# Kernel optimization log

Hardware: AMD Instinct MI355X
Metric: run time of the kernel (lower is better)

## Reference

```python
import jax, jax.numpy as jnp
import numpy as np

HIDDEN = 256
INPUT = 128
B, T = 256, 512
W_SCALE = 1.0 / np.sqrt(HIDDEN)  # matches PyTorch U(-1/sqrt(H), 1/sqrt(H)) magnitude


def setup_inputs() -> dict:
    key = jax.random.key(0)
    ks = jax.random.split(key, 5)
    x = jax.random.normal(ks[0], (B, T, INPUT), dtype=jnp.float32)
    W_ih = jax.random.normal(ks[1], (3 * HIDDEN, INPUT), dtype=jnp.float32) * W_SCALE
    W_hh = jax.random.normal(ks[2], (3 * HIDDEN, HIDDEN), dtype=jnp.float32) * W_SCALE
    b_ih = jax.random.normal(ks[3], (3 * HIDDEN,), dtype=jnp.float32) * W_SCALE
    b_hh = jax.random.normal(ks[4], (3 * HIDDEN,), dtype=jnp.float32) * W_SCALE
    return {"x": x, "W_ih": W_ih, "W_hh": W_hh, "b_ih": b_ih, "b_hh": b_hh}


def reference(x, W_ih, W_hh, b_ih, b_hh):
    # PyTorch GRU, gate order (r, z, n):
    #   r = sigmoid(W_ir x + b_ir + W_hr h + b_hr)
    #   z = sigmoid(W_iz x + b_iz + W_hz h + b_hz)
    #   n = tanh(W_in x + b_in + r * (W_hn h + b_hn))
    #   h' = (1 - z) * n + z * h
    Bsz = x.shape[0]
    H = W_hh.shape[1]
    # Precompute all input-to-gate projections once (big GEMM outside the scan).
    xg = jnp.einsum('bti,gi->btg', x, W_ih) + b_ih  # [B, T, 3H]

    def step(h, xg_t):
        hg = h @ W_hh.T + b_hh                      # [B, 3H]
        xr, xz, xn = jnp.split(xg_t, 3, axis=-1)
        hr, hz, hn = jnp.split(hg, 3, axis=-1)
        r = jax.nn.sigmoid(xr + hr)
        z = jax.nn.sigmoid(xz + hz)
        n = jnp.tanh(xn + r * hn)
        h_new = (1.0 - z) * n + z * h
        return h_new, h_new

    h0 = jnp.zeros((Bsz, H), dtype=x.dtype)
    _, hs = jax.lax.scan(step, h0, jnp.swapaxes(xg, 0, 1))  # hs: [T, B, H]
    return jnp.swapaxes(hs, 0, 1)                           # [B, T, H]
```

## Files before the change

### kernel.cpp

```cpp
#include <hip/hip_runtime.h>
#include <cstdint>
#include <cstddef>

typedef unsigned short u16;

#define HH 256
#define IIN 128
#define TT 512
#define G3 768

typedef __attribute__((ext_vector_type(8))) short bf16x8;
typedef __attribute__((ext_vector_type(4))) float f32x4;
typedef __attribute__((ext_vector_type(4))) int   i32x4;

__device__ __forceinline__ u16 f2bf(float f) {
    union { float f; uint32_t i; } c; c.f = f;
    uint32_t r = c.i + 0x7fffu + ((c.i >> 16) & 1u);
    return (u16)(r >> 16);
}
__device__ __forceinline__ float bf2f(u16 s) {
    union { uint32_t i; float f; } u; u.i = ((uint32_t)s) << 16; return u.f;
}
__device__ __forceinline__ float frcp(float x) { return __builtin_amdgcn_rcpf(x); }
__device__ __forceinline__ float sigm(float x) {
    float e = __expf(-fabsf(x));
    float s = frcp(1.f + e);
    return x >= 0.f ? s : 1.f - s;
}
__device__ __forceinline__ float tanh_f(float x) {
    float e = __expf(-2.f * fabsf(x));
    float t = (1.f - e) * frcp(1.f + e);
    return x >= 0.f ? t : -t;
}

#define LDS_BARRIER() asm volatile("s_waitcnt lgkmcnt(0)\n\ts_barrier" ::: "memory")

__global__ __launch_bounds__(512, 1) void xg_gemm(
    const float* __restrict__ x, const float* __restrict__ W_ih,
    const float* __restrict__ b_ih, const float* __restrict__ b_hh,
    u16* __restrict__ xg, int t0, int lt)
{
    __shared__ u16 wB[3][128 * 136];
    __shared__ float biasS[384];
    const int tid = threadIdx.x;
    const int TcM = (1 << lt) - 1;
    const int lane = tid & 63, wv = tid >> 6;
    const int quad = lane >> 4, colL = lane & 15;
    const int srow = tid >> 5, sc = (tid & 31) * 4;

    #pragma unroll
    for (int w3 = 0; w3 < 3; ++w3) {
        const int n0 = blockIdx.y * 384 + w3 * 128;
        #pragma unroll
        for (int it = 0; it < 8; ++it) {
            int r = srow + it * 16;
            float4 wv4 = *(const float4*)(W_ih + (size_t)(n0 + r) * IIN + sc);
            ushort4 ws4 = { f2bf(wv4.x), f2bf(wv4.y), f2bf(wv4.z), f2bf(wv4.w) };
            *(ushort4*)&wB[w3][r * 136 + sc] = ws4;
        }
    }
    if (tid < 384) {
        int g = blockIdx.y * 384 + tid;
        float bv = b_ih[g];
        if (g < 512) bv += b_hh[g];
        biasS[tid] = bv;
    }
    __syncthreads();

    const int colbase = blockIdx.y * 384;

    for (int p = 0; p < 4; ++p) {
        const int mrow = blockIdx.x * 1024 + p * 256 + wv * 32;

        bf16x8 A[2][4];
        #pragma unroll
        for (int i = 0; i < 2; ++i) {
            int row = mrow + i * 16 + colL;
            int b = row >> lt;
            int t = t0 + (row & TcM);
            const float* xr = x + ((size_t)b * TT + t) * IIN;
            #pragma unroll
            for (int kt = 0; kt < 4; ++kt) {
                float4 lo = *(const float4*)(xr + kt * 32 + quad * 8);
                float4 hi = *(const float4*)(xr + kt * 32 + quad * 8 + 4);
                union { bf16x8 v; u16 s[8]; } u;
                u.s[0] = f2bf(lo.x); u.s[1] = f2bf(lo.y);
                u.s[2] = f2bf(lo.z); u.s[3] = f2bf(lo.w);
                u.s[4] = f2bf(hi.x); u.s[5] = f2bf(hi.y);
                u.s[6] = f2bf(hi.z); u.s[7] = f2bf(hi.w);
                A[i][kt] = u.v;
            }
        }

        #pragma unroll
        for (int w3 = 0; w3 < 3; ++w3) {
            f32x4 C[2][8] = {};
            #pragma unroll
            for (int kt = 0; kt < 4; ++kt)
                #pragma unroll
                for (int nn = 0; nn < 8; ++nn) {
                    bf16x8 Bf = *(const bf16x8*)&wB[w3][(nn * 16 + colL) * 136 + kt * 32 + quad * 8];
                    C[0][nn] = __builtin_amdgcn_mfma_f32_16x16x32_bf16(A[0][kt], Bf, C[0][nn], 0, 0, 0);
                    C[1][nn] = __builtin_amdgcn_mfma_f32_16x16x32_bf16(A[1][kt], Bf, C[1][nn], 0, 0, 0);
                }
            #pragma unroll
            for (int i = 0; i < 2; ++i)
                #pragma unroll
                for (int nn = 0; nn < 8; ++nn) {
                    int cl = w3 * 128 + nn * 16 + colL;
                    float bv = biasS[cl];
                    #pragma unroll
                    for (int r = 0; r < 4; ++r) {
                        int row = mrow + i * 16 + quad * 4 + r;
                        xg[(size_t)row * G3 + colbase + cl] = f2bf(C[i][nn][r] + bv);
                    }
                }
        }
    }
}

#define GRU_STEP(TC_, HBR_, HBW_, HQR_, HQW_, PR_, PZ_, PN_) do {              \
    f32x4 Cn[2] = {};                                                          \
    i32x4 Cr[2] = {}, Cz[2] = {};                                              \
    _Pragma("unroll")                                                          \
    for (int kt = 0; kt < 4; ++kt) {                                           \
        i32x4 Aq = *(const i32x4*)((const char*)(HQR_) + kt * 64 + quad * 16); \
        Cr[0] = __builtin_amdgcn_mfma_i32_16x16x64_i8(Aq, Br[0][kt], Cr[0], 0, 0, 0); \
        Cr[1] = __builtin_amdgcn_mfma_i32_16x16x64_i8(Aq, Br[1][kt], Cr[1], 0, 0, 0); \
        Cz[0] = __builtin_amdgcn_mfma_i32_16x16x64_i8(Aq, Bz[0][kt], Cz[0], 0, 0, 0); \
        Cz[1] = __builtin_amdgcn_mfma_i32_16x16x64_i8(Aq, Bz[1][kt], Cz[1], 0, 0, 0); \
    }                                                                          \
    _Pragma("unroll")                                                          \
    for (int kt = 0; kt < 8; ++kt) {                                           \
        bf16x8 A = *(const bf16x8*)&HBR_[kt * 32 + quad * 8];                  \
        Cn[0] = __builtin_amdgcn_mfma_f32_16x16x32_bf16(A, Bn[0][kt], Cn[0], 0, 0, 0); \
        Cn[1] = __builtin_amdgcn_mfma_f32_16x16x32_bf16(A, Bn[1][kt], Cn[1], 0, 0, 0); \
    }                                                                          \
    float dr = (float)(i16 ? Cr[1][0] : Cr[0][0]) * scR;                       \
    float dz = (float)(i16 ? Cz[1][0] : Cz[0][0]) * scZ;                       \
    float dn = i16 ? Cn[1][0] : Cn[0][0];                                      \
    float xr = PR_, xz = PZ_, xn = PN_;                                        \
    int t2 = (TC_) + 2; if (t2 > Tc - 1) t2 = Tc - 1;                          \
    const u16* p2 = xgb + (size_t)t2 * G3;                                     \
    PR_ = bf2f(p2[j]); PZ_ = bf2f(p2[256 + j]); PN_ = bf2f(p2[512 + j]);       \
    float r = sigm(xr + dr);                                                   \
    float z = sigm(xz + dz);                                                   \
    float n = tanh_f(xn + r * (dn + bhn));                                     \
    hreg = n + z * (hreg - n);                                                 \
    float hc = fminf(fmaxf(hreg, -1.f), 1.f);       \
    int hq8 = (int)rintf(hc * 127.f);                                          \
    if (lane < 32) {                                                           \
        HBW_[j] = f2bf(hreg);                                                  \
        ((char*)(HQW_))[j] = (char)hq8;                                        \
        outb[(size_t)(t0 + (TC_)) * HH + j] = hreg;                            \
    }                                                                          \
    LDS_BARRIER();                                                             \
} while (0)

__global__ __launch_bounds__(512, 1) void gru_seq(
    const float* __restrict__ W_hh, const float* __restrict__ b_hh,
    const u16* __restrict__ xg, float* __restrict__ out,
    float* __restrict__ hstate, int t0, int Tc)
{
    __shared__ __align__(16) u16 hBuf[2][HH];
    __shared__ __align__(16) int hqBuf[2][HH / 4];

    const int tid = threadIdx.x;
    const int lane = tid & 63, wv = tid >> 6;
    const int quad = lane >> 4, colL = lane & 15;
    const int i16 = quad & 1;
    const int j = wv * 32 + (lane & 31);
    const int b = blockIdx.x;

    bf16x8 Bn[2][8];
    #pragma unroll
    for (int i = 0; i < 2; ++i) {
        const size_t rowb = (size_t)(512 + wv * 32 + i * 16 + colL) * HH;
        #pragma unroll
        for (int kt = 0; kt < 8; ++kt) {
            float4 lo = *(const float4*)(W_hh + rowb + kt * 32 + quad * 8);
            float4 hi = *(const float4*)(W_hh + rowb + kt * 32 + quad * 8 + 4);
            union { bf16x8 v; u16 s[8]; } u;
            u.s[0] = f2bf(lo.x); u.s[1] = f2bf(lo.y);
            u.s[2] = f2bf(lo.z); u.s[3] = f2bf(lo.w);
            u.s[4] = f2bf(hi.x); u.s[5] = f2bf(hi.y);
            u.s[6] = f2bf(hi.z); u.s[7] = f2bf(hi.w);
            Bn[i][kt] = u.v;
        }
    }

    i32x4 Br[2][4], Bz[2][4];
    float scR = 0.f, scZ = 0.f;
    #pragma unroll
    for (int g = 0; g < 2; ++g) {
        #pragma unroll
        for (int i = 0; i < 2; ++i) {
            const float* wr = W_hh + (size_t)(g * 256 + wv * 32 + i * 16 + colL) * HH;
            float m = 0.f;
            #pragma unroll
            for (int kt = 0; kt < 4; ++kt)
                #pragma unroll
                for (int u4 = 0; u4 < 4; ++u4) {
                    float4 v = *(const float4*)(wr + kt * 64 + quad * 16 + u4 * 4);
                    m = fmaxf(m, fmaxf(fmaxf(fabsf(v.x), fabsf(v.y)),
                                       fmaxf(fabsf(v.z), fabsf(v.w))));
                }
            m = fmaxf(m, __shfl_xor(m, 16));
            m = fmaxf(m, __shfl_xor(m, 32));
            float inv = m > 1e-30f ? 127.f / m : 0.f;
            float sc  = m * (1.f / 16129.f);
            #pragma unroll
            for (int kt = 0; kt < 4; ++kt) {
                int pk[4];
                #pragma unroll
                for (int u4 = 0; u4 < 4; ++u4) {
                    float4 v = *(const float4*)(wr + kt * 64 + quad * 16 + u4 * 4);
                    int q0 = (int)rintf(fminf(fmaxf(v.x * inv, -127.f), 127.f));
                    int q1 = (int)rintf(fminf(fmaxf(v.y * inv, -127.f), 127.f));
                    int q2 = (int)rintf(fminf(fmaxf(v.z * inv, -127.f), 127.f));
                    int q3 = (int)rintf(fminf(fmaxf(v.w * inv, -127.f), 127.f));
                    pk[u4] = (q0 & 255) | ((q1 & 255) << 8) | ((q2 & 255) << 16) | (q3 << 24);
                }
                i32x4 t = { pk[0], pk[1], pk[2], pk[3] };
                if (g == 0) Br[i][kt] = t; else Bz[i][kt] = t;
            }
            if (i == i16) { if (g == 0) scR = sc; else scZ = sc; }
        }
    }

    float hreg = (t0 == 0) ? 0.f : hstate[b * HH + j];
    if (lane < 32) {
        hBuf[0][j] = f2bf(hreg);
        float hc = fminf(fmaxf(hreg, -1.f), 1.f);
        ((char*)hqBuf[0])[j] = (char)(int)rintf(hc * 127.f);
    }
    const float bhn = b_hh[512 + j];
    const u16* xgb = xg + (size_t)b * Tc * G3;
    float* outb = out + (size_t)b * TT * HH;

    float pr0 = bf2f(xgb[j]),      pz0 = bf2f(xgb[256 + j]),      pn0 = bf2f(xgb[512 + j]);
    float pr1 = bf2f(xgb[G3 + j]), pz1 = bf2f(xgb[G3 + 256 + j]), pn1 = bf2f(xgb[G3 + 512 + j]);
    __syncthreads();

    for (int tc = 0; tc < Tc; tc += 2) {
        GRU_STEP(tc,     hBuf[0], hBuf[1], hqBuf[0], hqBuf[1], pr0, pz0, pn0);
        GRU_STEP(tc + 1, hBuf[1], hBuf[0], hqBuf[1], hqBuf[0], pr1, pz1, pn1);
    }

    if (t0 + Tc < TT && lane < 32)
        hstate[b * HH + j] = hreg;
}

extern "C" void kernel_launch(void* const* d_in, const int* in_sizes, int n_in,
                              void* d_out, int out_size, void* d_ws, size_t ws_size,
                              hipStream_t stream) {
    const float* x    = (const float*)d_in[0];
    const float* W_ih = (const float*)d_in[1];
    const float* W_hh = (const float*)d_in[2];
    const float* b_ih = (const float*)d_in[3];
    const float* b_hh = (const float*)d_in[4];
    float* out = (float*)d_out;

    float* hstate = (float*)d_ws;
    u16* xg = (u16*)((char*)d_ws + 262144);
    size_t avail = ws_size > 262144 ? ws_size - 262144 : 0;

    int Tc = TT, lt = 9;
    while (Tc > 4 && (size_t)256 * Tc * G3 * 2 > avail) { Tc >>= 1; --lt; }

    for (int t0 = 0; t0 < TT; t0 += Tc) {
        xg_gemm<<<dim3(Tc / 4, 2), 512, 0, stream>>>(
            x, W_ih, b_ih, b_hh, xg, t0, lt);
        gru_seq<<<dim3(256), 512, 0, stream>>>(
            W_hh, b_hh, xg, out, hstate, t0, Tc);
    }
}
```

Before: 713.1 us.

## Fuse input-projection GEMM into per-batch GRU recurrence kernel

Removes the separate xg_gemm launch and has each per-batch GRU block compute its own input projections. The block stages its x slice in LDS as bf16 and keeps a 96-column slice of W_ih per wave in registers. Results are written to that block's private xg region before the recurrence reads them back. This saves one kernel launch per chunk and improves cache locality for xg, but the GEMM now runs on only 256 blocks (one per batch) rather than a wide grid. It also adds about 139 KB of LDS and extra register pressure to the serial kernel.

```diff
diff --git a/kernel.cpp b/kernel.cpp
--- a/kernel.cpp
+++ b/kernel.cpp
@@ -34,90 +34,6 @@
 }
 
 #define LDS_BARRIER() asm volatile("s_waitcnt lgkmcnt(0)\n\ts_barrier" ::: "memory")
-
-__global__ __launch_bounds__(512, 1) void xg_gemm(
-    const float* __restrict__ x, const float* __restrict__ W_ih,
-    const float* __restrict__ b_ih, const float* __restrict__ b_hh,
-    u16* __restrict__ xg, int t0, int lt)
-{
-    __shared__ u16 wB[3][128 * 136];
-    __shared__ float biasS[384];
-    const int tid = threadIdx.x;
-    const int TcM = (1 << lt) - 1;
-    const int lane = tid & 63, wv = tid >> 6;
-    const int quad = lane >> 4, colL = lane & 15;
-    const int srow = tid >> 5, sc = (tid & 31) * 4;
-
-    #pragma unroll
-    for (int w3 = 0; w3 < 3; ++w3) {
-        const int n0 = blockIdx.y * 384 + w3 * 128;
-        #pragma unroll
-        for (int it = 0; it < 8; ++it) {
-            int r = srow + it * 16;
-            float4 wv4 = *(const float4*)(W_ih + (size_t)(n0 + r) * IIN + sc);
-            ushort4 ws4 = { f2bf(wv4.x), f2bf(wv4.y), f2bf(wv4.z), f2bf(wv4.w) };
-            *(ushort4*)&wB[w3][r * 136 + sc] = ws4;
-        }
-    }
-    if (tid < 384) {
-        int g = blockIdx.y * 384 + tid;
-        float bv = b_ih[g];
-        if (g < 512) bv += b_hh[g];
-        biasS[tid] = bv;
-    }
-    __syncthreads();
-
-    const int colbase = blockIdx.y * 384;
-
-    for (int p = 0; p < 4; ++p) {
-        const int mrow = blockIdx.x * 1024 + p * 256 + wv * 32;
-
-        bf16x8 A[2][4];
-        #pragma unroll
-        for (int i = 0; i < 2; ++i) {
-            int row = mrow + i * 16 + colL;
-            int b = row >> lt;
-            int t = t0 + (row & TcM);
-            const float* xr = x + ((size_t)b * TT + t) * IIN;
-            #pragma unroll
-            for (int kt = 0; kt < 4; ++kt) {
-                float4 lo = *(const float4*)(xr + kt * 32 + quad * 8);
-                float4 hi = *(const float4*)(xr + kt * 32 + quad * 8 + 4);
-                union { bf16x8 v; u16 s[8]; } u;
-                u.s[0] = f2bf(lo.x); u.s[1] = f2bf(lo.y);
-                u.s[2] = f2bf(lo.z); u.s[3] = f2bf(lo.w);
-                u.s[4] = f2bf(hi.x); u.s[5] = f2bf(hi.y);
-                u.s[6] = f2bf(hi.z); u.s[7] = f2bf(hi.w);
-                A[i][kt] = u.v;
-            }
-        }
-
-        #pragma unroll
-        for (int w3 = 0; w3 < 3; ++w3) {
-            f32x4 C[2][8] = {};
-            #pragma unroll
-            for (int kt = 0; kt < 4; ++kt)
-                #pragma unroll
-                for (int nn = 0; nn < 8; ++nn) {
-                    bf16x8 Bf = *(const bf16x8*)&wB[w3][(nn * 16 + colL) * 136 + kt * 32 + quad * 8];
-                    C[0][nn] = __builtin_amdgcn_mfma_f32_16x16x32_bf16(A[0][kt], Bf, C[0][nn], 0, 0, 0);
-                    C[1][nn] = __builtin_amdgcn_mfma_f32_16x16x32_bf16(A[1][kt], Bf, C[1][nn], 0, 0, 0);
-                }
-            #pragma unroll
-            for (int i = 0; i < 2; ++i)
-                #pragma unroll
-                for (int nn = 0; nn < 8; ++nn) {
-                    int cl = w3 * 128 + nn * 16 + colL;
-                    float bv = biasS[cl];
-                    #pragma unroll
-                    for (int r = 0; r < 4; ++r) {
-                        int row = mrow + i * 16 + quad * 4 + r;
-                        xg[(size_t)row * G3 + colbase + cl] = f2bf(C[i][nn][r] + bv);
-                    }
-                }
-        }
-    }
-}
 
 #define GRU_STEP(TC_, HBR_, HBW_, HQR_, HQW_, PR_, PZ_, PN_) do {              \
     f32x4 Cn[2] = {};                                                          \
@@ -157,11 +73,14 @@
     LDS_BARRIER();                                                             \
 } while (0)
 
-__global__ __launch_bounds__(512, 1) void gru_seq(
-    const float* __restrict__ W_hh, const float* __restrict__ b_hh,
-    const u16* __restrict__ xg, float* __restrict__ out,
+__global__ __launch_bounds__(512, 1) void gru_fused(
+    const float* __restrict__ x, const float* __restrict__ W_ih,
+    const float* __restrict__ W_hh,
+    const float* __restrict__ b_ih, const float* __restrict__ b_hh,
+    u16* __restrict__ xg, float* __restrict__ out,
     float* __restrict__ hstate, int t0, int Tc)
 {
+    __shared__ u16 xS[TT * 136];
     __shared__ __align__(16) u16 hBuf[2][HH];
     __shared__ __align__(16) int hqBuf[2][HH / 4];
 
@@ -171,6 +90,63 @@
     const int i16 = quad & 1;
     const int j = wv * 32 + (lane & 31);
     const int b = blockIdx.x;
+
+    u16* xgw = xg + (size_t)b * Tc * G3;
+
+    {
+        for (int idx = tid; idx < Tc * 32; idx += 512) {
+            int r = idx >> 5, c4 = (idx & 31) * 4;
+            float4 xv = *(const float4*)(x + ((size_t)b * TT + t0 + r) * IIN + c4);
+            ushort4 xs = { f2bf(xv.x), f2bf(xv.y), f2bf(xv.z), f2bf(xv.w) };
+            *(ushort4*)&xS[r * 136 + c4] = xs;
+        }
+        bf16x8 Bi[6][4];
+        float bvv[6];
+        #pragma unroll
+        for (int n = 0; n < 6; ++n) {
+            int col = wv * 96 + n * 16 + colL;
+            const float* wr = W_ih + (size_t)col * IIN;
+            #pragma unroll
+            for (int kt = 0; kt < 4; ++kt) {
+                float4 lo = *(const float4*)(wr + kt * 32 + quad * 8);
+                float4 hi = *(const float4*)(wr + kt * 32 + quad * 8 + 4);
+                union { bf16x8 v; u16 s[8]; } u;
+                u.s[0] = f2bf(lo.x); u.s[1] = f2bf(lo.y);
+                u.s[2] = f2bf(lo.z); u.s[3] = f2bf(lo.w);
+                u.s[4] = f2bf(hi.x); u.s[5] = f2bf(hi.y);
+                u.s[6] = f2bf(hi.z); u.s[7] = f2bf(hi.w);
+                Bi[n][kt] = u.v;
+            }
+            float bv = b_ih[col];
+            if (col < 512) bv += b_hh[col];
+            bvv[n] = bv;
+        }
+        __syncthreads();
+
+        for (int mt = 0; mt < Tc / 16; ++mt) {
+            bf16x8 A[4];
+            #pragma unroll
+            for (int kt = 0; kt < 4; ++kt)
+                A[kt] = *(const bf16x8*)&xS[(mt * 16 + colL) * 136 + kt * 32 + quad * 8];
+            f32x4 C[6] = {};
+            #pragma unroll
+            for (int kt = 0; kt < 4; ++kt)
+                #pragma unroll
+                for (int n = 0; n < 6; ++n)
+                    C[n] = __builtin_amdgcn_mfma_f32_16x16x32_bf16(A[kt], Bi[n][kt], C[n], 0, 0, 0);
+            #pragma unroll
+            for (int n = 0; n < 6; ++n) {
+                int col = wv * 96 + n * 16 + colL;
+                #pragma unroll
+                for (int r = 0; r < 4; ++r) {
+                    int tt = mt * 16 + quad * 4 + r;
+                    xgw[(size_t)tt * G3 + col] = f2bf(C[n][r] + bvv[n]);
+                }
+            }
+        }
+        asm volatile("s_waitcnt vmcnt(0)" ::: "memory");
+        __syncthreads();
+    }
 
     bf16x8 Bn[2][8];
     #pragma unroll
@@ -235,7 +211,7 @@
         ((char*)hqBuf[0])[j] = (char)(int)rintf(hc * 127.f);
     }
     const float bhn = b_hh[512 + j];
-    const u16* xgb = xg + (size_t)b * Tc * G3;
+    const u16* xgb = xgw;
     float* outb = out + (size_t)b * TT * HH;
 
     float pr0 = bf2f(xgb[j]),      pz0 = bf2f(xgb[256 + j]),      pn0 = bf2f(xgb[512 + j]);
@@ -265,13 +241,11 @@
     u16* xg = (u16*)((char*)d_ws + 262144);
     size_t avail = ws_size > 262144 ? ws_size - 262144 : 0;
 
-    int Tc = TT, lt = 9;
-    while (Tc > 4 && (size_t)256 * Tc * G3 * 2 > avail) { Tc >>= 1; --lt; }
+    int Tc = TT;
+    while (Tc > 16 && (size_t)256 * Tc * G3 * 2 > avail) Tc >>= 1;
 
     for (int t0 = 0; t0 < TT; t0 += Tc) {
-        xg_gemm<<<dim3(Tc / 4, 2), 512, 0, stream>>>(
-            x, W_ih, b_ih, b_hh, xg, t0, lt);
-        gru_seq<<<dim3(256), 512, 0, stream>>>(
-            W_hh, b_hh, xg, out, hstate, t0, Tc);
-    }
-}
+        gru_fused<<<dim3(256), 512, 0, stream>>>(
+            x, W_ih, W_hh, b_ih, b_hh, xg, out, hstate, t0, Tc);
+    }
+}
```

After: 682.0 us. -4.4%, faster.
